# Kernel optimization log

Hardware: AMD Instinct MI355X
Metric: run time of the kernel (lower is better)

## Reference

```python
import jax, jax.numpy as jnp
import numpy as np
import math

B, S, D, H = 2, 2048, 1024, 16
D_K = D // H


def setup_inputs() -> dict:
    key = jax.random.key(0)
    ks = jax.random.split(key, 9)
    scale = 0.02
    return {
        "query": jax.random.normal(ks[0], (B, S, D), dtype=jnp.float32),
        "key": jax.random.normal(ks[1], (B, S, D), dtype=jnp.float32),
        "value": jax.random.normal(ks[2], (B, S, D), dtype=jnp.float32),
        "padding_mask": jax.random.bernoulli(ks[3], 0.1, (B, 1, 1, S)),
        "Wq": jax.random.normal(ks[4], (D, D), dtype=jnp.float32) * scale,
        "bq": jnp.zeros((D,), dtype=jnp.float32),
        "Wk": jax.random.normal(ks[5], (D, D), dtype=jnp.float32) * scale,
        "bk": jnp.zeros((D,), dtype=jnp.float32),
        "Wv": jax.random.normal(ks[6], (D, D), dtype=jnp.float32) * scale,
        "bv": jnp.zeros((D,), dtype=jnp.float32),
        "Wo": jax.random.normal(ks[7], (D, D), dtype=jnp.float32) * scale,
        "bo": jnp.zeros((D,), dtype=jnp.float32),
    }


def reference(query, key, value, padding_mask, Wq, bq, Wk, bk, Wv, bv, Wo, bo):
    # projections -> [B, H, S, d_k]
    q = (query @ Wq + bq).reshape(B, S, H, D_K).transpose(0, 2, 1, 3)
    k = (key @ Wk + bk).reshape(B, S, H, D_K).transpose(0, 2, 1, 3)
    v = (value @ Wv + bv).reshape(B, S, H, D_K).transpose(0, 2, 1, 3)

    # scores: [B, H, S, S]
    scores = jnp.einsum("bhqd,bhkd->bhqk", q, k) / math.sqrt(D_K)

    # faithful to original: triu(scores, 1).bool() -> True where upper-tri score != 0,
    # masked positions get value 1e-10 (NOT -inf) before softmax
    causal_mask = jnp.triu(scores, k=1) != 0
    scores = jnp.where(causal_mask, jnp.float32(1e-10), scores)
    scores = jnp.where(padding_mask, jnp.float32(1e-10), scores)

    attn = jax.nn.softmax(scores, axis=-1)
    out = jnp.einsum("bhqk,bhkd->bhqd", attn, v)  # [B, H, S, d_k]
    out = out.transpose(0, 2, 1, 3).reshape(B, S, D)
    return out @ Wo + bo
```

## Files before the change

### kernel.cpp

```cpp
#include <hip/hip_runtime.h>
#include <hip/hip_bf16.h>
#include <cstdint>
#include <cstddef>

typedef __hip_bfloat16 bf16;
typedef __attribute__((ext_vector_type(8))) short short8;
typedef __attribute__((ext_vector_type(4))) short s4v;
typedef __attribute__((ext_vector_type(4))) float floatx4;

#define B_ 2
#define S_ 2048
#define D_ 1024
#define H_ 16
#define DK_ 64
#define M_ 4096
#define HEADELEMS 131072
#define TILEELEMS 4096
#define QSCALE 0.1803368801111204f

struct __align__(8) bf16x4 { bf16 x, y, z, w; };

__device__ __forceinline__ floatx4 mfma16(short8 a, short8 b, floatx4 c) {
  return __builtin_amdgcn_mfma_f32_16x16x32_bf16(a, b, c, 0, 0, 0);
}
__device__ __forceinline__ void gl_lds16(const bf16* g, bf16* l) {
  __builtin_amdgcn_global_load_lds((const __attribute__((address_space(1))) void*)g,
                                   (__attribute__((address_space(3))) void*)l, 16, 0, 0);
}
__device__ __forceinline__ float bs2f(short s) {
  bf16 b = *reinterpret_cast<bf16*>(&s);
  return __bfloat162float(b);
}
__device__ __forceinline__ s4v pack4(float p0, float p1, float p2, float p3) {
  union { __hip_bfloat162 h; short2 s; } ua, ub;
  ua.h = __float22bfloat162_rn(make_float2(p0, p1));
  ub.h = __float22bfloat162_rn(make_float2(p2, p3));
  s4v r = {ua.s.x, ua.s.y, ub.s.x, ub.s.y};
  return r;
}
__device__ __forceinline__ float fast_exp2(float x) {
#if __has_builtin(__builtin_amdgcn_exp2f)
  return __builtin_amdgcn_exp2f(x);
#else
  float r; asm("v_exp_f32 %0, %1" : "=v"(r) : "v"(x)); return r;
#endif
}

__global__ void prep_kernel(const float* __restrict__ q_in, const float* __restrict__ k_in,
                            const float* __restrict__ v_in,
                            const float* __restrict__ Wq, const float* __restrict__ Wk,
                            const float* __restrict__ Wv, const float* __restrict__ Wo,
                            bf16* __restrict__ xq, bf16* __restrict__ xk, bf16* __restrict__ xv,
                            bf16* __restrict__ wqt, bf16* __restrict__ wkt,
                            bf16* __restrict__ wvt, bf16* __restrict__ wot,
                            const unsigned int* __restrict__ pmask, int* __restrict__ flag) {
  __shared__ bf16 tile[64][66];
  __shared__ int sbyte;
  const int blk = blockIdx.x;
  const int tid = threadIdx.x;
  if (blk < 12288) {
    const int z = blk >> 12;
    const int i = ((blk & 4095) << 8) | tid;
    const float* src = (z == 0) ? q_in : (z == 1) ? k_in : v_in;
    bf16* dst = (z == 0) ? xq : (z == 1) ? xk : xv;
    float4 v = ((const float4*)src)[i];
    bf16x4 o = { __float2bfloat16(v.x), __float2bfloat16(v.y),
                 __float2bfloat16(v.z), __float2bfloat16(v.w) };
    ((bf16x4*)dst)[i] = o;
  } else if (blk < 13312) {
    const int t = blk - 12288;
    const int z = t >> 8;
    const int rc = t & 255;
    const int r0 = (rc >> 4) * 64, c0 = (rc & 15) * 64;
    const float* src = (z == 0) ? Wq : (z == 1) ? Wk : (z == 2) ? Wv : Wo;
    bf16* dst = (z == 0) ? wqt : (z == 1) ? wkt : (z == 2) ? wvt : wot;
    const int lr = tid >> 4;
    const int lc4 = (tid & 15) * 4;
#pragma unroll
    for (int i = 0; i < 4; ++i) {
      const int r = lr + i * 16;
      float4 v = *(const float4*)(src + (size_t)(r0 + r) * D_ + c0 + lc4);
      tile[r][lc4 + 0] = __float2bfloat16(v.x);
      tile[r][lc4 + 1] = __float2bfloat16(v.y);
      tile[r][lc4 + 2] = __float2bfloat16(v.z);
      tile[r][lc4 + 3] = __float2bfloat16(v.w);
    }
    __syncthreads();
    const int orr = tid & 63;
    const int oc0 = tid >> 6;
#pragma unroll
    for (int j = 0; j < 16; ++j) {
      const int oc = oc0 + j * 4;
      dst[(size_t)(c0 + oc) * D_ + r0 + orr] = tile[orr][oc];
    }
  } else {
    if (tid == 0) sbyte = 0;
    __syncthreads();
    for (int i = tid; i < (B_ * S_) / 4; i += 256) {
      const unsigned int v = pmask[i];
      if (((v & 0xFEFEFEFEu) == 0u) && ((v & 0xFFFFFF00u) != 0u)) sbyte = 1;
    }
    __syncthreads();
    if (tid == 0) *flag = sbyte;
  }
}

template<int MT>
__global__ __launch_bounds__(256, 2) void gemm_k(
    const bf16* __restrict__ A0, const bf16* __restrict__ A1, const bf16* __restrict__ A2,
    const bf16* __restrict__ W0, const bf16* __restrict__ W1, const bf16* __restrict__ W2,
    const float* __restrict__ b0, const float* __restrict__ b1, const float* __restrict__ b2,
    void* __restrict__ O0, void* __restrict__ O1, void* __restrict__ O2,
    const int mode01, const int Kd, const float sc)
{
  constexpr int ROWS = MT + 128;
  __shared__ __align__(16) bf16 sh[2 * ROWS * 64];
  const int z = blockIdx.z;
  const bf16* A = (z == 0) ? A0 : (z == 1) ? A1 : A2;
  const bf16* W = (z == 0) ? W0 : (z == 1) ? W1 : W2;
  const float* bias = (z == 0) ? b0 : (z == 1) ? b1 : b2;
  void* Cout = (z == 0) ? O0 : (z == 1) ? O1 : O2;
  const int mode = (z == 2) ? 1 : mode01;
  const float scz = (z == 0) ? sc : 1.f;

  constexpr int MI = MT / 32;
  const int tid = threadIdx.x;
  const int wave = tid >> 6, lane = tid & 63;
  const int quad = lane >> 4, lc = lane & 15;
  const int wm = (wave >> 1) * (MT / 2), wn = (wave & 1) * 64;
  const int m0 = blockIdx.x * MT, n0 = blockIdx.y * 128;

  const floatx4 zero4 = {0.f, 0.f, 0.f, 0.f};
  floatx4 acc[MI][4];
#pragma unroll
  for (int mi = 0; mi < MI; ++mi)
#pragma unroll
    for (int ni = 0; ni < 4; ++ni) acc[mi][ni] = zero4;

  const int srow = lane >> 3;
  const int schunk = ((lane & 7) ^ srow) * 8;
  const bf16* Ag = A + (size_t)(m0 + wave * (MT / 4) + srow) * Kd + schunk;
  const bf16* Bg = W + (size_t)(n0 + wave * 32 + srow) * Kd + schunk;

  auto stage = [&](bf16* buf, int k0) {
    bf16* As0 = buf + wave * (MT / 4) * 64;
    bf16* Bs0 = buf + MT * 64 + wave * 32 * 64;
#pragma unroll
    for (int j = 0; j < MT / 32; ++j)
      gl_lds16(Ag + k0 + (size_t)(j * 8) * Kd, As0 + j * 512);
#pragma unroll
    for (int j = 0; j < 4; ++j)
      gl_lds16(Bg + k0 + (size_t)(j * 8) * Kd, Bs0 + j * 512);
  };

  stage(sh, 0);
  asm volatile("s_waitcnt vmcnt(0)" ::: "memory");
  __syncthreads();

  int cur = 0;
  for (int k0 = 0; k0 < Kd; k0 += 64) {
    bf16* cbuf = cur ? sh + ROWS * 64 : sh;
    bf16* nbuf = cur ? sh : sh + ROWS * 64;
    const bool more = (k0 + 64 < Kd);
    if (more) stage(nbuf, k0 + 64);

    const bf16* Ar = cbuf;
    const bf16* Br = cbuf + MT * 64;
    short8 af[2][MI], bfr[2][4];
#pragma unroll
    for (int kk = 0; kk < 2; ++kk) {
#pragma unroll
      for (int i = 0; i < MI; ++i)
        af[kk][i] = *(const short8*)(Ar + (wm + i * 16 + lc) * 64
                                     + (((kk * 4 + quad) ^ (lc & 7)) * 8));
#pragma unroll
      for (int i = 0; i < 4; ++i)
        bfr[kk][i] = *(const short8*)(Br + (wn + i * 16 + lc) * 64
                                      + (((kk * 4 + quad) ^ (lc & 7)) * 8));
    }
#pragma unroll
    for (int kk = 0; kk < 2; ++kk)
#pragma unroll
      for (int mi = 0; mi < MI; ++mi)
#pragma unroll
        for (int ni = 0; ni < 4; ++ni)
          acc[mi][ni] = mfma16(af[kk][mi], bfr[kk][ni], acc[mi][ni]);

    __syncthreads();
    cur ^= 1;
  }

  if (mode == 2) {
    float* out = (float*)Cout;
#pragma unroll
    for (int mi = 0; mi < MI; ++mi)
#pragma unroll
      for (int ni = 0; ni < 4; ++ni) {
        const int col = n0 + wn + ni * 16 + lc;
        const float bv = bias[col];
        const int rbase = m0 + wm + mi * 16 + quad * 4;
#pragma unroll
        for (int r = 0; r < 4; ++r)
          out[(size_t)(rbase + r) * D_ + col] = acc[mi][ni][r] + bv;
      }
  } else {
    bf16* pool = sh + wave * 2048;
    float bvs[4];
#pragma unroll
    for (int ni = 0; ni < 4; ++ni) bvs[ni] = bias[n0 + wn + ni * 16 + lc];
    const int hcol = (n0 + wn) >> 6;
    const int mglob = m0 + wm;
    bf16* outb = (bf16*)Cout + (size_t)((mglob >> 11) * H_ + hcol) * HEADELEMS
               + (size_t)((mglob & (S_ - 1)) >> 6) * TILEELEMS;
#pragma unroll
    for (int half = 0; half < MI / 2; ++half) {
#pragma unroll
      for (int mi2 = 0; mi2 < 2; ++mi2) {
        const int mi = half * 2 + mi2;
#pragma unroll
        for (int ni = 0; ni < 4; ++ni) {
          const int dkl = ni * 16 + lc;
#pragma unroll
          for (int r = 0; r < 4; ++r) {
            const float v = (acc[mi][ni][r] + bvs[ni]) * scz;
            int idx;
            if (mode == 0) {
              const int c = (mi2 * 2 + (dkl >> 5)) * 64 + ((dkl >> 3) & 3) * 16 + quad * 4 + r;
              idx = c * 8 + (dkl & 7);
            } else {
              const int c = (mi2 * 4 + (dkl >> 4)) * 64 + quad * 16 + (dkl & 15);
              idx = c * 4 + r;
            }
            pool[idx] = __float2bfloat16(v);
          }
        }
      }
#pragma unroll
      for (int t = 0; t < 4; ++t) {
        const short8 vv = *(const short8*)(pool + t * 512 + lane * 8);
        *(short8*)(outb + half * 2048 + t * 512 + lane * 8) = vv;
      }
    }
  }
}

__global__ void suf_kernel(const bf16* __restrict__ vp, float* __restrict__ suf) {
  __shared__ float ts[32 * 64];
  const int bhid = blockIdx.x;
  const bf16* vb = vp + (size_t)bhid * HEADELEMS;
  const int tid = threadIdx.x;
  const int dk = tid & 63, g = tid >> 6;
  const int dkt = dk >> 4, lck = dk & 15;
  for (int T = g * 8; T < g * 8 + 8; ++T) {
    float sum = 0.f;
#pragma unroll
    for (int w = 0; w < 4; ++w)
#pragma unroll
      for (int qd = 0; qd < 4; ++qd) {
        const s4v x = *(const s4v*)(vb + (size_t)T * TILEELEMS
                                    + (size_t)(((w * 4 + dkt) * 64 + qd * 16 + lck)) * 4);
        sum += bs2f(x[0]) + bs2f(x[1]) + bs2f(x[2]) + bs2f(x[3]);
      }
    ts[T * 64 + dk] = sum;
  }
  __syncthreads();
  if (g == 0) {
    float run = 0.f;
    float* out = suf + (size_t)bhid * (33 * 64);
    out[32 * 64 + dk] = 0.f;
    for (int T = 31; T >= 0; --T) { run += ts[T * 64 + dk]; out[T * 64 + dk] = run; }
  }
}

template<bool DIAGP>
__device__ __forceinline__ void qk_tile(const short8 ak0, const short8 ak1,
                                        const short8 (&qf)[4][2],
                                        const unsigned int (&pmb)[4], const int T,
                                        float (&lacc)[4], s4v (&pf)[4],
                                        const int w, const int quad, const int lc,
                                        const bool diag) {
  const floatx4 z4 = {0.f, 0.f, 0.f, 0.f};
  const short ONE = (short)0x3F80;
#pragma unroll
  for (int qt = 0; qt < 4; ++qt) {
    if (DIAGP && diag && w > qt) {
      s4v o1 = {ONE, ONE, ONE, ONE};
      pf[qt] = o1;
      lacc[qt] += 4.f;
      continue;
    }
    floatx4 s = mfma16(ak0, qf[qt][0], z4);
    s = mfma16(ak1, qf[qt][1], s);
    float pv[4];
#pragma unroll
    for (int r = 0; r < 4; ++r) {
      bool m = ((pmb[r] >> T) & 1u) != 0u;
      if (DIAGP && diag && w == qt) m = m || (quad * 4 + r > lc);
      pv[r] = fast_exp2(m ? 0.f : s[r]);
      lacc[qt] += pv[r];
    }
    pf[qt] = pack4(pv[0], pv[1], pv[2], pv[3]);
  }
}

__device__ __forceinline__ void pv_step(const s4v (&va0)[4], const s4v (&va1)[4],
                                        const s4v (&pf0)[4], const s4v (&pf1)[4],
                                        floatx4 (&oacc)[4][4]) {
  short8 pB[4];
#pragma unroll
  for (int qt = 0; qt < 4; ++qt)
    pB[qt] = __builtin_shufflevector(pf0[qt], pf1[qt], 0, 1, 2, 3, 4, 5, 6, 7);
#pragma unroll
  for (int dkt = 0; dkt < 4; ++dkt) {
    const short8 av = __builtin_shufflevector(va0[dkt], va1[dkt], 0, 1, 2, 3, 4, 5, 6, 7);
#pragma unroll
    for (int qt = 0; qt < 4; ++qt)
      oacc[dkt][qt] = mfma16(av, pB[qt], oacc[dkt][qt]);
  }
}

__device__ __forceinline__ void stage8(const bf16* kb, const bf16* vb, bf16* slot,
                                       const int T0, const int T1,
                                       const int wl, const int wreg) {
  const bf16* k0 = kb + (size_t)T0 * TILEELEMS + wl;
  const bf16* k1 = kb + (size_t)T1 * TILEELEMS + wl;
  const bf16* v0 = vb + (size_t)T0 * TILEELEMS + wl;
  const bf16* v1 = vb + (size_t)T1 * TILEELEMS + wl;
  gl_lds16(k0,       slot + wreg);
  gl_lds16(k0 + 512, slot + wreg + 512);
  gl_lds16(k1,       slot + 4096 + wreg);
  gl_lds16(k1 + 512, slot + 4096 + wreg + 512);
  gl_lds16(v0,       slot + 8192 + wreg);
  gl_lds16(v0 + 512, slot + 8192 + wreg + 512);
  gl_lds16(v1,       slot + 12288 + wreg);
  gl_lds16(v1 + 512, slot + 12288 + wreg + 512);
}

__global__ __launch_bounds__(256, 1) void attn_kernel(
    const bf16* __restrict__ qp, const bf16* __restrict__ kp,
    const bf16* __restrict__ vp, const float* __restrict__ suf,
    const void* __restrict__ pad, const int* __restrict__ flag,
    bf16* __restrict__ oa)
{
  __shared__ __align__(16) bf16 lds[32768];

  const int lin = blockIdx.x;
  const int xcd = lin & 7;
  const int t = lin >> 3;
  const int grp = t >> 4;
  const int jq = t & 15;
  const int bh = xcd + 8 * grp;
  const int b = bh >> 4, h = bh & 15;

  const int tid = threadIdx.x;
  const int w = tid >> 6, lane = tid & 63, quad = lane >> 4, lc = lane & 15;
  const int bytemode = *flag;

  const int wreg = w * 1024;
  const int wl = wreg + lane * 8;
  const int vl = wreg + lane * 4;

  const bf16* kb = kp + (size_t)bh * HEADELEMS;
  const bf16* vb = vp + (size_t)bh * HEADELEMS;

  unsigned int pmb[4] = {0u, 0u, 0u, 0u};
  if (bytemode) {
    const unsigned char* pp = (const unsigned char*)pad + b * S_ + w * 16 + quad * 4;
#pragma unroll
    for (int T = 0; T < 32; ++T) {
      const uchar4 u = *(const uchar4*)(pp + T * 64);
      pmb[0] |= (u.x ? 1u : 0u) << T;
      pmb[1] |= (u.y ? 1u : 0u) << T;
      pmb[2] |= (u.z ? 1u : 0u) << T;
      pmb[3] |= (u.w ? 1u : 0u) << T;
    }
  } else {
    const int* pp = (const int*)pad + b * S_ + w * 16 + quad * 4;
#pragma unroll
    for (int T = 0; T < 32; ++T) {
      const int4 u = *(const int4*)(pp + (size_t)T * 64);
      pmb[0] |= (u.x ? 1u : 0u) << T;
      pmb[1] |= (u.y ? 1u : 0u) << T;
      pmb[2] |= (u.z ? 1u : 0u) << T;
      pmb[3] |= (u.w ? 1u : 0u) << T;
    }
  }

#pragma unroll 1
  for (int qsel = 0; qsel < 2; ++qsel) {
    const int myqt = qsel ? jq : 31 - jq;
    const int mynt = myqt + 1;
    const int np = (mynt + 1) >> 1;

    const bf16* qb = qp + (size_t)bh * HEADELEMS + (size_t)myqt * TILEELEMS;
    gl_lds16(qb + wl,       lds + 16384 + wreg);
    gl_lds16(qb + wl + 512, lds + 16384 + wreg + 512);
    stage8(kb, vb, lds, 0, 1, wl, wreg);
    asm volatile("s_waitcnt vmcnt(0)" ::: "memory");
    __syncthreads();

    short8 qf[4][2];
#pragma unroll
    for (int qt = 0; qt < 4; ++qt)
#pragma unroll
      for (int hh = 0; hh < 2; ++hh)
        qf[qt][hh] = *(const short8*)(lds + 16384 + qt * 1024 + hh * 512 + lane * 8);
    __syncthreads();

    const floatx4 zero4 = {0.f, 0.f, 0.f, 0.f};
    floatx4 oacc[4][4];
#pragma unroll
    for (int i = 0; i < 4; ++i)
#pragma unroll
      for (int jj = 0; jj < 4; ++jj) oacc[i][jj] = zero4;
    float lacc[4] = {0.f, 0.f, 0.f, 0.f};

#pragma unroll 1
    for (int p = 0; p < np; ++p) {
      if (p + 1 < np) {
        stage8(kb, vb, lds + (((p + 1) & 1) << 14), 2 * p + 2, 2 * p + 3, wl, wreg);
        asm volatile("s_waitcnt vmcnt(8)" ::: "memory");
      } else {
        asm volatile("s_waitcnt vmcnt(0)" ::: "memory");
      }
      __builtin_amdgcn_sched_barrier(0);

      bf16* slot = lds + ((p & 1) << 14);
      const short8 ak00 = *(const short8*)(slot + wl);
      const short8 ak01 = *(const short8*)(slot + wl + 512);
      const short8 ak10 = *(const short8*)(slot + 4096 + wl);
      const short8 ak11 = *(const short8*)(slot + 4096 + wl + 512);
      s4v va0[4], va1[4];
#pragma unroll
      for (int dkt = 0; dkt < 4; ++dkt) {
        va0[dkt] = *(const s4v*)(slot + 8192 + vl + dkt * 256);
        va1[dkt] = *(const s4v*)(slot + 12288 + vl + dkt * 256);
      }

      const int T0 = 2 * p, T1 = 2 * p + 1;
      s4v pf0[4], pf1[4];
      if (p + 1 < np) {
        qk_tile<false>(ak00, ak01, qf, pmb, T0, lacc, pf0, w, quad, lc, false);
        qk_tile<false>(ak10, ak11, qf, pmb, T1, lacc, pf1, w, quad, lc, false);
      } else {
        qk_tile<true>(ak00, ak01, qf, pmb, T0, lacc, pf0, w, quad, lc, T0 == mynt - 1);
        if (T1 < mynt) {
          qk_tile<true>(ak10, ak11, qf, pmb, T1, lacc, pf1, w, quad, lc, true);
        } else {
          const s4v zz = {0, 0, 0, 0};
#pragma unroll
          for (int qt = 0; qt < 4; ++qt) pf1[qt] = zz;
        }
      }
      pv_step(va0, va1, pf0, pf1, oacc);
    }

    __syncthreads();

    float* fbuf = (float*)lds;
    bf16* obuf = lds + 8704;
    float* lbuf = (float*)(lds + 13312);

#pragma unroll
    for (int qt = 0; qt < 4; ++qt) {
      float v = lacc[qt];
      v += __shfl_xor(v, 16);
      v += __shfl_xor(v, 32);
      if (quad == 0) lbuf[w * 64 + qt * 16 + lc] = v;
    }
    __syncthreads();
    float ls = lbuf[0 * 64 + w * 16 + lc] + lbuf[1 * 64 + w * 16 + lc]
             + lbuf[2 * 64 + w * 16 + lc] + lbuf[3 * 64 + w * 16 + lc];
    ls += (float)(S_ - mynt * 64);
    const float linv = 1.f / ls;
    const float* sufp = suf + (size_t)bh * (33 * 64) + mynt * 64;

#pragma unroll
    for (int dktG = 0; dktG < 4; ++dktG) {
#pragma unroll
      for (int qt = 0; qt < 4; ++qt) {
        const floatx4 a = oacc[dktG][qt];
        float* dst = fbuf + (w * 4 + qt) * 272 + lc;
#pragma unroll
        for (int r = 0; r < 4; ++r) dst[(quad * 4 + r) * 17] = a[r];
      }
      __syncthreads();
      const float4 sv4 = *(const float4*)(sufp + dktG * 16 + quad * 4);
      float v[4];
#pragma unroll
      for (int r = 0; r < 4; ++r) {
        const int e = (quad * 4 + r) * 17 + lc;
        v[r] = fbuf[(0 * 4 + w) * 272 + e] + fbuf[(1 * 4 + w) * 272 + e]
             + fbuf[(2 * 4 + w) * 272 + e] + fbuf[(3 * 4 + w) * 272 + e];
      }
      v[0] = (v[0] + sv4.x) * linv; v[1] = (v[1] + sv4.y) * linv;
      v[2] = (v[2] + sv4.z) * linv; v[3] = (v[3] + sv4.w) * linv;
      bf16x4 pk = { __float2bfloat16(v[0]), __float2bfloat16(v[1]),
                    __float2bfloat16(v[2]), __float2bfloat16(v[3]) };
      *(bf16x4*)(obuf + (w * 16 + lc) * 72 + dktG * 16 + quad * 4) = pk;
      __syncthreads();
    }

    const size_t obase = (size_t)(b * S_ + myqt * 64) * D_ + h * 64;
#pragma unroll
    for (int it = 0; it < 2; ++it) {
      const int idx = it * 256 + tid;
      const int row = idx >> 3, c8 = (idx & 7) * 8;
      const short8 vv = *(const short8*)(obuf + row * 72 + c8);
      *(short8*)(oa + obase + (size_t)row * D_ + c8) = vv;
    }
    __syncthreads();
  }
}

extern "C" void kernel_launch(void* const* d_in, const int* in_sizes, int n_in,
                              void* d_out, int out_size, void* d_ws, size_t ws_size,
                              hipStream_t stream) {
  (void)in_sizes; (void)n_in; (void)out_size; (void)ws_size;
  const float* q_in = (const float*)d_in[0];
  const float* k_in = (const float*)d_in[1];
  const float* v_in = (const float*)d_in[2];
  const void*  pmask = d_in[3];
  const float* Wq = (const float*)d_in[4];
  const float* bq = (const float*)d_in[5];
  const float* Wk = (const float*)d_in[6];
  const float* bk = (const float*)d_in[7];
  const float* Wv = (const float*)d_in[8];
  const float* bv = (const float*)d_in[9];
  const float* Wo = (const float*)d_in[10];
  const float* bo = (const float*)d_in[11];

  char* ws = (char*)d_ws;
  bf16* xq  = (bf16*)(ws + 0);
  bf16* xk  = (bf16*)(ws + 8388608);
  bf16* xv  = (bf16*)(ws + 16777216);
  bf16* wqt = (bf16*)(ws + 25165824);
  bf16* wkt = (bf16*)(ws + 27262976);
  bf16* wvt = (bf16*)(ws + 29360128);
  bf16* wot = (bf16*)(ws + 31457280);
  bf16* qpp = (bf16*)(ws + 33554432);
  bf16* kpp = (bf16*)(ws + 41943040);
  bf16* vpp = (bf16*)(ws + 50331648);
  float* suf = (float*)(ws + 25165824);
  int*  flg = (int*)(ws + 58720256);
  bf16* oa  = xq;

  prep_kernel<<<13313, 256, 0, stream>>>(q_in, k_in, v_in, Wq, Wk, Wv, Wo,
                                         xq, xk, xv, wqt, wkt, wvt, wot,
                                         (const unsigned int*)pmask, flg);

  gemm_k<128><<<dim3(32, 8, 3), 256, 0, stream>>>(xq, xk, xv, wqt, wkt, wvt,
                                                  bq, bk, bv, qpp, kpp, vpp, 0, D_, QSCALE);
  suf_kernel<<<32, 256, 0, stream>>>(vpp, suf);

  attn_kernel<<<512, 256, 0, stream>>>(qpp, kpp, vpp, suf, pmask, flg, oa);

  gemm_k<128><<<dim3(32, 8, 1), 256, 0, stream>>>(oa, oa, oa, wot, wot, wot,
                                                  bo, bo, bo, d_out, d_out, d_out, 2, D_, 1.f);
}
```

Measured before the change: 216.3 us.

## Compute softmax row sums via MFMA and split K/V waits in attention loop

Replaces the per-lane scalar accumulation of softmax denominators with an extra MFMA against a ones vector, so the sums fall out of the matrix unit and the cross-lane shuffles at the end go away. The P tile is built directly in the MFMA operand layout instead of being shuffled together afterwards. The wait on staged loads is split so QK^T can start once the K tiles arrive while the V tiles are still in flight. Launch bounds now allow two blocks per CU, which may constrain register allocation. Masked entries now map directly to one instead of exp2(0).

```diff
diff --git a/kernel.cpp b/kernel.cpp
--- a/kernel.cpp
+++ b/kernel.cpp
@@ -276,17 +276,19 @@
 __device__ __forceinline__ void qk_tile(const short8 ak0, const short8 ak1,
                                         const short8 (&qf)[4][2],
                                         const unsigned int (&pmb)[4], const int T,
-                                        float (&lacc)[4], s4v (&pf)[4],
+                                        short8 (&pB)[4], const int half,
                                         const int w, const int quad, const int lc,
                                         const bool diag) {
   const floatx4 z4 = {0.f, 0.f, 0.f, 0.f};
   const short ONE = (short)0x3F80;
+  bool mm[4];
+#pragma unroll
+  for (int r = 0; r < 4; ++r) mm[r] = ((pmb[r] >> T) & 1u) != 0u;
 #pragma unroll
   for (int qt = 0; qt < 4; ++qt) {
     if (DIAGP && diag && w > qt) {
       s4v o1 = {ONE, ONE, ONE, ONE};
-      pf[qt] = o1;
-      lacc[qt] += 4.f;
+      ((s4v*)&pB[qt])[half] = o1;
       continue;
     }
     floatx4 s = mfma16(ak0, qf[qt][0], z4);
@@ -294,29 +296,24 @@
     float pv[4];
 #pragma unroll
     for (int r = 0; r < 4; ++r) {
-      bool m = ((pmb[r] >> T) & 1u) != 0u;
+      bool m = mm[r];
       if (DIAGP && diag && w == qt) m = m || (quad * 4 + r > lc);
-      pv[r] = fast_exp2(m ? 0.f : s[r]);
-      lacc[qt] += pv[r];
-    }
-    pf[qt] = pack4(pv[0], pv[1], pv[2], pv[3]);
-  }
-}
-
-__device__ __forceinline__ void pv_step(const s4v (&va0)[4], const s4v (&va1)[4],
-                                        const s4v (&pf0)[4], const s4v (&pf1)[4],
+      pv[r] = m ? 1.f : fast_exp2(s[r]);
+    }
+    ((s4v*)&pB[qt])[half] = pack4(pv[0], pv[1], pv[2], pv[3]);
+  }
+}
+
+__device__ __forceinline__ void pv_step(const short8 (&av)[4], const short8 (&pB)[4],
+                                        const short8 ones, floatx4 (&lsum)[4],
                                         floatx4 (&oacc)[4][4]) {
-  short8 pB[4];
-#pragma unroll
-  for (int qt = 0; qt < 4; ++qt)
-    pB[qt] = __builtin_shufflevector(pf0[qt], pf1[qt], 0, 1, 2, 3, 4, 5, 6, 7);
-#pragma unroll
-  for (int dkt = 0; dkt < 4; ++dkt) {
-    const short8 av = __builtin_shufflevector(va0[dkt], va1[dkt], 0, 1, 2, 3, 4, 5, 6, 7);
+#pragma unroll
+  for (int qt = 0; qt < 4; ++qt) lsum[qt] = mfma16(ones, pB[qt], lsum[qt]);
+#pragma unroll
+  for (int dkt = 0; dkt < 4; ++dkt)
 #pragma unroll
     for (int qt = 0; qt < 4; ++qt)
-      oacc[dkt][qt] = mfma16(av, pB[qt], oacc[dkt][qt]);
-  }
+      oacc[dkt][qt] = mfma16(av[dkt], pB[qt], oacc[dkt][qt]);
 }
 
 __device__ __forceinline__ void stage8(const bf16* kb, const bf16* vb, bf16* slot,
@@ -336,7 +333,7 @@
   gl_lds16(v1 + 512, slot + 12288 + wreg + 512);
 }
 
-__global__ __launch_bounds__(256, 1) void attn_kernel(
+__global__ __launch_bounds__(256, 2) void attn_kernel(
     const bf16* __restrict__ qp, const bf16* __restrict__ kp,
     const bf16* __restrict__ vp, const float* __restrict__ suf,
     const void* __restrict__ pad, const int* __restrict__ flag,
@@ -363,6 +360,9 @@
   const bf16* kb = kp + (size_t)bh * HEADELEMS;
   const bf16* vb = vp + (size_t)bh * HEADELEMS;
 
+  const short ONE = (short)0x3F80;
+  const short8 ones = {ONE, ONE, ONE, ONE, ONE, ONE, ONE, ONE};
+
   unsigned int pmb[4] = {0u, 0u, 0u, 0u};
   if (bytemode) {
     const unsigned char* pp = (const unsigned char*)pad + b * S_ + w * 16 + quad * 4;
@@ -413,15 +413,16 @@
     for (int i = 0; i < 4; ++i)
 #pragma unroll
       for (int jj = 0; jj < 4; ++jj) oacc[i][jj] = zero4;
-    float lacc[4] = {0.f, 0.f, 0.f, 0.f};
+    floatx4 lsum[4] = {zero4, zero4, zero4, zero4};
 
 #pragma unroll 1
     for (int p = 0; p < np; ++p) {
-      if (p + 1 < np) {
+      const bool more = (p + 1 < np);
+      if (more) {
         stage8(kb, vb, lds + (((p + 1) & 1) << 14), 2 * p + 2, 2 * p + 3, wl, wreg);
-        asm volatile("s_waitcnt vmcnt(8)" ::: "memory");
+        asm volatile("s_waitcnt vmcnt(12)" ::: "memory");
       } else {
-        asm volatile("s_waitcnt vmcnt(0)" ::: "memory");
+        asm volatile("s_waitcnt vmcnt(4)" ::: "memory");
       }
       __builtin_amdgcn_sched_barrier(0);
 
@@ -430,29 +431,34 @@
       const short8 ak01 = *(const short8*)(slot + wl + 512);
       const short8 ak10 = *(const short8*)(slot + 4096 + wl);
       const short8 ak11 = *(const short8*)(slot + 4096 + wl + 512);
-      s4v va0[4], va1[4];
-#pragma unroll
-      for (int dkt = 0; dkt < 4; ++dkt) {
-        va0[dkt] = *(const s4v*)(slot + 8192 + vl + dkt * 256);
-        va1[dkt] = *(const s4v*)(slot + 12288 + vl + dkt * 256);
-      }
 
       const int T0 = 2 * p, T1 = 2 * p + 1;
-      s4v pf0[4], pf1[4];
-      if (p + 1 < np) {
-        qk_tile<false>(ak00, ak01, qf, pmb, T0, lacc, pf0, w, quad, lc, false);
-        qk_tile<false>(ak10, ak11, qf, pmb, T1, lacc, pf1, w, quad, lc, false);
+      short8 pB[4];
+      if (more) {
+        qk_tile<false>(ak00, ak01, qf, pmb, T0, pB, 0, w, quad, lc, false);
+        qk_tile<false>(ak10, ak11, qf, pmb, T1, pB, 1, w, quad, lc, false);
       } else {
-        qk_tile<true>(ak00, ak01, qf, pmb, T0, lacc, pf0, w, quad, lc, T0 == mynt - 1);
+        qk_tile<true>(ak00, ak01, qf, pmb, T0, pB, 0, w, quad, lc, T0 == mynt - 1);
         if (T1 < mynt) {
-          qk_tile<true>(ak10, ak11, qf, pmb, T1, lacc, pf1, w, quad, lc, true);
+          qk_tile<true>(ak10, ak11, qf, pmb, T1, pB, 1, w, quad, lc, true);
         } else {
           const s4v zz = {0, 0, 0, 0};
 #pragma unroll
-          for (int qt = 0; qt < 4; ++qt) pf1[qt] = zz;
+          for (int qt = 0; qt < 4; ++qt) ((s4v*)&pB[qt])[1] = zz;
         }
       }
-      pv_step(va0, va1, pf0, pf1, oacc);
+
+      if (more) asm volatile("s_waitcnt vmcnt(8)" ::: "memory");
+      else      asm volatile("s_waitcnt vmcnt(0)" ::: "memory");
+      __builtin_amdgcn_sched_barrier(0);
+
+      short8 av[4];
+#pragma unroll
+      for (int dkt = 0; dkt < 4; ++dkt) {
+        ((s4v*)&av[dkt])[0] = *(const s4v*)(slot + 8192 + vl + dkt * 256);
+        ((s4v*)&av[dkt])[1] = *(const s4v*)(slot + 12288 + vl + dkt * 256);
+      }
+      pv_step(av, pB, ones, lsum, oacc);
     }
 
     __syncthreads();
@@ -462,12 +468,8 @@
     float* lbuf = (float*)(lds + 13312);
 
 #pragma unroll
-    for (int qt = 0; qt < 4; ++qt) {
-      float v = lacc[qt];
-      v += __shfl_xor(v, 16);
-      v += __shfl_xor(v, 32);
-      if (quad == 0) lbuf[w * 64 + qt * 16 + lc] = v;
-    }
+    for (int qt = 0; qt < 4; ++qt)
+      if (quad == 0) lbuf[w * 64 + qt * 16 + lc] = lsum[qt][0];
     __syncthreads();
     float ls = lbuf[0 * 64 + w * 16 + lc] + lbuf[1 * 64 + w * 16 + lc]
              + lbuf[2 * 64 + w * 16 + lc] + lbuf[3 * 64 + w * 16 + lc];
```

Result: slower. 221.4 us (+2.4%).

## Split attention block into 8 waves with per-tile 4-stage K/V pipeline

Applied to the files above, without the earlier changes.

The attention kernel goes from 256 to 512 threads per block. Each wave now owns one key sub-tile and half of the query tiles, which halves the per-wave accumulator state. Staging changes from two-tile double buffering to a 4-slot ring of single 64-key tiles: half the waves load K and half load V, and PV MFMAs run on pairs of tiles. The aim is more waves in flight to hide latency and lower register pressure, at the cost of more barriers per tile and a reworked reduction epilogue.

```diff
diff --git a/kernel.cpp b/kernel.cpp
--- a/kernel.cpp
+++ b/kernel.cpp
@@ -19,6 +19,7 @@
 #define QSCALE 0.1803368801111204f
 
 struct __align__(8) bf16x4 { bf16 x, y, z, w; };
+struct __align__(4) bf16x2 { bf16 x, y; };
 
 __device__ __forceinline__ floatx4 mfma16(short8 a, short8 b, floatx4 c) {
   return __builtin_amdgcn_mfma_f32_16x16x32_bf16(a, b, c, 0, 0, 0);
@@ -213,10 +214,10 @@
     bf16* outb = (bf16*)Cout + (size_t)((mglob >> 11) * H_ + hcol) * HEADELEMS
                + (size_t)((mglob & (S_ - 1)) >> 6) * TILEELEMS;
 #pragma unroll
-    for (int half = 0; half < MI / 2; ++half) {
+    for (int half2 = 0; half2 < MI / 2; ++half2) {
 #pragma unroll
       for (int mi2 = 0; mi2 < 2; ++mi2) {
-        const int mi = half * 2 + mi2;
+        const int mi = half2 * 2 + mi2;
 #pragma unroll
         for (int ni = 0; ni < 4; ++ni) {
           const int dkl = ni * 16 + lc;
@@ -238,7 +239,7 @@
 #pragma unroll
       for (int t = 0; t < 4; ++t) {
         const short8 vv = *(const short8*)(pool + t * 512 + lane * 8);
-        *(short8*)(outb + half * 2048 + t * 512 + lane * 8) = vv;
+        *(short8*)(outb + half2 * 2048 + t * 512 + lane * 8) = vv;
       }
     }
   }
@@ -273,19 +274,20 @@
 }
 
 template<bool DIAGP>
-__device__ __forceinline__ void qk_tile(const short8 ak0, const short8 ak1,
-                                        const short8 (&qf)[4][2],
-                                        const unsigned int (&pmb)[4], const int T,
-                                        float (&lacc)[4], s4v (&pf)[4],
-                                        const int w, const int quad, const int lc,
-                                        const bool diag) {
+__device__ __forceinline__ void qk2(const short8 ak0, const short8 ak1,
+                                    const short8 (&qf)[2][2],
+                                    const unsigned int (&pmb)[4], const int T,
+                                    short8 (&pB)[2], float (&lacc)[2], const int hlf,
+                                    const int kw, const int qh,
+                                    const int quad, const int lc, const bool diag) {
   const floatx4 z4 = {0.f, 0.f, 0.f, 0.f};
   const short ONE = (short)0x3F80;
 #pragma unroll
-  for (int qt = 0; qt < 4; ++qt) {
-    if (DIAGP && diag && w > qt) {
+  for (int qt = 0; qt < 2; ++qt) {
+    const int qtg = qh * 2 + qt;
+    if (DIAGP && diag && kw > qtg) {
       s4v o1 = {ONE, ONE, ONE, ONE};
-      pf[qt] = o1;
+      ((s4v*)&pB[qt])[hlf] = o1;
       lacc[qt] += 4.f;
       continue;
     }
@@ -295,48 +297,15 @@
 #pragma unroll
     for (int r = 0; r < 4; ++r) {
       bool m = ((pmb[r] >> T) & 1u) != 0u;
-      if (DIAGP && diag && w == qt) m = m || (quad * 4 + r > lc);
-      pv[r] = fast_exp2(m ? 0.f : s[r]);
+      if (DIAGP && diag && kw == qtg) m = m || (quad * 4 + r > lc);
+      pv[r] = m ? 1.f : fast_exp2(s[r]);
       lacc[qt] += pv[r];
     }
-    pf[qt] = pack4(pv[0], pv[1], pv[2], pv[3]);
-  }
-}
-
-__device__ __forceinline__ void pv_step(const s4v (&va0)[4], const s4v (&va1)[4],
-                                        const s4v (&pf0)[4], const s4v (&pf1)[4],
-                                        floatx4 (&oacc)[4][4]) {
-  short8 pB[4];
-#pragma unroll
-  for (int qt = 0; qt < 4; ++qt)
-    pB[qt] = __builtin_shufflevector(pf0[qt], pf1[qt], 0, 1, 2, 3, 4, 5, 6, 7);
-#pragma unroll
-  for (int dkt = 0; dkt < 4; ++dkt) {
-    const short8 av = __builtin_shufflevector(va0[dkt], va1[dkt], 0, 1, 2, 3, 4, 5, 6, 7);
-#pragma unroll
-    for (int qt = 0; qt < 4; ++qt)
-      oacc[dkt][qt] = mfma16(av, pB[qt], oacc[dkt][qt]);
-  }
-}
-
-__device__ __forceinline__ void stage8(const bf16* kb, const bf16* vb, bf16* slot,
-                                       const int T0, const int T1,
-                                       const int wl, const int wreg) {
-  const bf16* k0 = kb + (size_t)T0 * TILEELEMS + wl;
-  const bf16* k1 = kb + (size_t)T1 * TILEELEMS + wl;
-  const bf16* v0 = vb + (size_t)T0 * TILEELEMS + wl;
-  const bf16* v1 = vb + (size_t)T1 * TILEELEMS + wl;
-  gl_lds16(k0,       slot + wreg);
-  gl_lds16(k0 + 512, slot + wreg + 512);
-  gl_lds16(k1,       slot + 4096 + wreg);
-  gl_lds16(k1 + 512, slot + 4096 + wreg + 512);
-  gl_lds16(v0,       slot + 8192 + wreg);
-  gl_lds16(v0 + 512, slot + 8192 + wreg + 512);
-  gl_lds16(v1,       slot + 12288 + wreg);
-  gl_lds16(v1 + 512, slot + 12288 + wreg + 512);
-}
-
-__global__ __launch_bounds__(256, 1) void attn_kernel(
+    ((s4v*)&pB[qt])[hlf] = pack4(pv[0], pv[1], pv[2], pv[3]);
+  }
+}
+
+__global__ __launch_bounds__(512, 4) void attn_kernel(
     const bf16* __restrict__ qp, const bf16* __restrict__ kp,
     const bf16* __restrict__ vp, const float* __restrict__ suf,
     const void* __restrict__ pad, const int* __restrict__ flag,
@@ -354,18 +323,18 @@
 
   const int tid = threadIdx.x;
   const int w = tid >> 6, lane = tid & 63, quad = lane >> 4, lc = lane & 15;
+  const int kw = w & 3, qh = w >> 2;
   const int bytemode = *flag;
-
-  const int wreg = w * 1024;
-  const int wl = wreg + lane * 8;
-  const int vl = wreg + lane * 4;
 
   const bf16* kb = kp + (size_t)bh * HEADELEMS;
   const bf16* vb = vp + (size_t)bh * HEADELEMS;
+  const bf16* stgsrc = qh ? vb : kb;
+  const int stgoff = kw * 1024;
+  const int stgdst = (qh ? 4096 : 0) + kw * 1024;
 
   unsigned int pmb[4] = {0u, 0u, 0u, 0u};
   if (bytemode) {
-    const unsigned char* pp = (const unsigned char*)pad + b * S_ + w * 16 + quad * 4;
+    const unsigned char* pp = (const unsigned char*)pad + b * S_ + kw * 16 + quad * 4;
 #pragma unroll
     for (int T = 0; T < 32; ++T) {
       const uchar4 u = *(const uchar4*)(pp + T * 64);
@@ -375,7 +344,7 @@
       pmb[3] |= (u.w ? 1u : 0u) << T;
     }
   } else {
-    const int* pp = (const int*)pad + b * S_ + w * 16 + quad * 4;
+    const int* pp = (const int*)pad + b * S_ + kw * 16 + quad * 4;
 #pragma unroll
     for (int T = 0; T < 32; ++T) {
       const int4 u = *(const int4*)(pp + (size_t)T * 64);
@@ -390,69 +359,88 @@
   for (int qsel = 0; qsel < 2; ++qsel) {
     const int myqt = qsel ? jq : 31 - jq;
     const int mynt = myqt + 1;
-    const int np = (mynt + 1) >> 1;
 
     const bf16* qb = qp + (size_t)bh * HEADELEMS + (size_t)myqt * TILEELEMS;
-    gl_lds16(qb + wl,       lds + 16384 + wreg);
-    gl_lds16(qb + wl + 512, lds + 16384 + wreg + 512);
-    stage8(kb, vb, lds, 0, 1, wl, wreg);
-    asm volatile("s_waitcnt vmcnt(0)" ::: "memory");
-    __syncthreads();
-
-    short8 qf[4][2];
-#pragma unroll
-    for (int qt = 0; qt < 4; ++qt)
+    bf16* qarea = lds + 3 * 8192;
+    gl_lds16(qb + w * 512 + lane * 8, qarea + w * 512);
+    {
+      const bf16* s0 = stgsrc + stgoff + lane * 8;
+      gl_lds16(s0, lds + stgdst);
+      gl_lds16(s0 + 512, lds + stgdst + 512);
+      if (mynt > 1) {
+        const bf16* s1 = stgsrc + (size_t)TILEELEMS + stgoff + lane * 8;
+        gl_lds16(s1, lds + 8192 + stgdst);
+        gl_lds16(s1 + 512, lds + 8192 + stgdst + 512);
+      }
+    }
+    if (mynt > 1) asm volatile("s_waitcnt vmcnt(4)" ::: "memory");
+    else          asm volatile("s_waitcnt vmcnt(2)" ::: "memory");
+    __builtin_amdgcn_s_barrier();
+    __builtin_amdgcn_sched_barrier(0);
+
+    short8 qf[2][2];
+#pragma unroll
+    for (int qt = 0; qt < 2; ++qt)
 #pragma unroll
       for (int hh = 0; hh < 2; ++hh)
-        qf[qt][hh] = *(const short8*)(lds + 16384 + qt * 1024 + hh * 512 + lane * 8);
-    __syncthreads();
+        qf[qt][hh] = *(const short8*)(qarea + (qh * 2 + qt) * 1024 + hh * 512 + lane * 8);
+    asm volatile("s_waitcnt lgkmcnt(0)" ::: "memory");
+    __builtin_amdgcn_sched_barrier(0);
+    __builtin_amdgcn_s_barrier();
 
     const floatx4 zero4 = {0.f, 0.f, 0.f, 0.f};
-    floatx4 oacc[4][4];
+    floatx4 oacc[4][2];
 #pragma unroll
     for (int i = 0; i < 4; ++i)
 #pragma unroll
-      for (int jj = 0; jj < 4; ++jj) oacc[i][jj] = zero4;
-    float lacc[4] = {0.f, 0.f, 0.f, 0.f};
+      for (int jj = 0; jj < 2; ++jj) oacc[i][jj] = zero4;
+    float lacc[2] = {0.f, 0.f};
+    short8 pB[2];
 
 #pragma unroll 1
-    for (int p = 0; p < np; ++p) {
-      if (p + 1 < np) {
-        stage8(kb, vb, lds + (((p + 1) & 1) << 14), 2 * p + 2, 2 * p + 3, wl, wreg);
-        asm volatile("s_waitcnt vmcnt(8)" ::: "memory");
-      } else {
-        asm volatile("s_waitcnt vmcnt(0)" ::: "memory");
-      }
+    for (int T = 0; T < mynt; ++T) {
+      if (T + 1 < mynt) asm volatile("s_waitcnt vmcnt(2)" ::: "memory");
+      else              asm volatile("s_waitcnt vmcnt(0)" ::: "memory");
+      __builtin_amdgcn_s_barrier();
       __builtin_amdgcn_sched_barrier(0);
 
-      bf16* slot = lds + ((p & 1) << 14);
-      const short8 ak00 = *(const short8*)(slot + wl);
-      const short8 ak01 = *(const short8*)(slot + wl + 512);
-      const short8 ak10 = *(const short8*)(slot + 4096 + wl);
-      const short8 ak11 = *(const short8*)(slot + 4096 + wl + 512);
-      s4v va0[4], va1[4];
-#pragma unroll
-      for (int dkt = 0; dkt < 4; ++dkt) {
-        va0[dkt] = *(const s4v*)(slot + 8192 + vl + dkt * 256);
-        va1[dkt] = *(const s4v*)(slot + 12288 + vl + dkt * 256);
-      }
-
-      const int T0 = 2 * p, T1 = 2 * p + 1;
-      s4v pf0[4], pf1[4];
-      if (p + 1 < np) {
-        qk_tile<false>(ak00, ak01, qf, pmb, T0, lacc, pf0, w, quad, lc, false);
-        qk_tile<false>(ak10, ak11, qf, pmb, T1, lacc, pf1, w, quad, lc, false);
-      } else {
-        qk_tile<true>(ak00, ak01, qf, pmb, T0, lacc, pf0, w, quad, lc, T0 == mynt - 1);
-        if (T1 < mynt) {
-          qk_tile<true>(ak10, ak11, qf, pmb, T1, lacc, pf1, w, quad, lc, true);
-        } else {
+      if (T + 2 < mynt) {
+        bf16* sl = lds + (((T + 2) & 3) << 13) + stgdst;
+        const bf16* src = stgsrc + (size_t)(T + 2) * TILEELEMS + stgoff + lane * 8;
+        gl_lds16(src, sl);
+        gl_lds16(src + 512, sl + 512);
+      }
+
+      const bf16* slot = lds + ((T & 3) << 13);
+      const short8 ak0 = *(const short8*)(slot + kw * 1024 + lane * 8);
+      const short8 ak1 = *(const short8*)(slot + kw * 1024 + 512 + lane * 8);
+
+      const int hlf = T & 1;
+      const bool diag = (T == mynt - 1);
+      if (!diag) qk2<false>(ak0, ak1, qf, pmb, T, pB, lacc, hlf, kw, qh, quad, lc, false);
+      else       qk2<true >(ak0, ak1, qf, pmb, T, pB, lacc, hlf, kw, qh, quad, lc, true);
+
+      if (hlf == 1 || diag) {
+        if (diag && hlf == 0) {
           const s4v zz = {0, 0, 0, 0};
 #pragma unroll
-          for (int qt = 0; qt < 4; ++qt) pf1[qt] = zz;
+          for (int qt = 0; qt < 2; ++qt) ((s4v*)&pB[qt])[1] = zz;
         }
-      }
-      pv_step(va0, va1, pf0, pf1, oacc);
+        const int Te = T & ~1;
+        const bf16* se = lds + ((Te & 3) << 13);
+        const bf16* so = (hlf == 1) ? slot : se;
+        short8 av[4];
+#pragma unroll
+        for (int dkt = 0; dkt < 4; ++dkt) {
+          ((s4v*)&av[dkt])[0] = *(const s4v*)(se + 4096 + kw * 1024 + dkt * 256 + lane * 4);
+          ((s4v*)&av[dkt])[1] = *(const s4v*)(so + 4096 + kw * 1024 + dkt * 256 + lane * 4);
+        }
+#pragma unroll
+        for (int dkt = 0; dkt < 4; ++dkt)
+#pragma unroll
+          for (int qt = 0; qt < 2; ++qt)
+            oacc[dkt][qt] = mfma16(av[dkt], pB[qt], oacc[dkt][qt]);
+      }
     }
 
     __syncthreads();
@@ -462,15 +450,17 @@
     float* lbuf = (float*)(lds + 13312);
 
 #pragma unroll
-    for (int qt = 0; qt < 4; ++qt) {
+    for (int qt = 0; qt < 2; ++qt) {
       float v = lacc[qt];
       v += __shfl_xor(v, 16);
       v += __shfl_xor(v, 32);
-      if (quad == 0) lbuf[w * 64 + qt * 16 + lc] = v;
-    }
-    __syncthreads();
-    float ls = lbuf[0 * 64 + w * 16 + lc] + lbuf[1 * 64 + w * 16 + lc]
-             + lbuf[2 * 64 + w * 16 + lc] + lbuf[3 * 64 + w * 16 + lc];
+      if (quad == 0) lbuf[(qh * 2 + qt) * 64 + kw * 16 + lc] = v;
+    }
+    __syncthreads();
+    const int qtgR = w & 3;
+    const int rh = w >> 2;
+    float ls = lbuf[qtgR * 64 + 0 * 16 + lc] + lbuf[qtgR * 64 + 1 * 16 + lc]
+             + lbuf[qtgR * 64 + 2 * 16 + lc] + lbuf[qtgR * 64 + 3 * 16 + lc];
     ls += (float)(S_ - mynt * 64);
     const float linv = 1.f / ls;
     const float* sufp = suf + (size_t)bh * (33 * 64) + mynt * 64;
@@ -478,34 +468,31 @@
 #pragma unroll
     for (int dktG = 0; dktG < 4; ++dktG) {
 #pragma unroll
-      for (int qt = 0; qt < 4; ++qt) {
+      for (int qt = 0; qt < 2; ++qt) {
         const floatx4 a = oacc[dktG][qt];
-        float* dst = fbuf + (w * 4 + qt) * 272 + lc;
+        float* dst = fbuf + (qh * 2 + qt) * 1088 + kw * 272 + lc;
 #pragma unroll
         for (int r = 0; r < 4; ++r) dst[(quad * 4 + r) * 17] = a[r];
       }
       __syncthreads();
-      const float4 sv4 = *(const float4*)(sufp + dktG * 16 + quad * 4);
-      float v[4];
-#pragma unroll
-      for (int r = 0; r < 4; ++r) {
-        const int e = (quad * 4 + r) * 17 + lc;
-        v[r] = fbuf[(0 * 4 + w) * 272 + e] + fbuf[(1 * 4 + w) * 272 + e]
-             + fbuf[(2 * 4 + w) * 272 + e] + fbuf[(3 * 4 + w) * 272 + e];
-      }
-      v[0] = (v[0] + sv4.x) * linv; v[1] = (v[1] + sv4.y) * linv;
-      v[2] = (v[2] + sv4.z) * linv; v[3] = (v[3] + sv4.w) * linv;
-      bf16x4 pk = { __float2bfloat16(v[0]), __float2bfloat16(v[1]),
-                    __float2bfloat16(v[2]), __float2bfloat16(v[3]) };
-      *(bf16x4*)(obuf + (w * 16 + lc) * 72 + dktG * 16 + quad * 4) = pk;
+      const float2 sv = *(const float2*)(sufp + dktG * 16 + rh * 8 + quad * 2);
+      float v0, v1;
+      {
+        const int e0 = qtgR * 1088 + (rh * 8 + quad * 2 + 0) * 17 + lc;
+        const int e1 = qtgR * 1088 + (rh * 8 + quad * 2 + 1) * 17 + lc;
+        v0 = fbuf[e0] + fbuf[e0 + 272] + fbuf[e0 + 544] + fbuf[e0 + 816];
+        v1 = fbuf[e1] + fbuf[e1 + 272] + fbuf[e1 + 544] + fbuf[e1 + 816];
+      }
+      v0 = (v0 + sv.x) * linv;
+      v1 = (v1 + sv.y) * linv;
+      bf16x2 pk = { __float2bfloat16(v0), __float2bfloat16(v1) };
+      *(bf16x2*)(obuf + (qtgR * 16 + lc) * 72 + dktG * 16 + rh * 8 + quad * 2) = pk;
       __syncthreads();
     }
 
     const size_t obase = (size_t)(b * S_ + myqt * 64) * D_ + h * 64;
-#pragma unroll
-    for (int it = 0; it < 2; ++it) {
-      const int idx = it * 256 + tid;
-      const int row = idx >> 3, c8 = (idx & 7) * 8;
+    {
+      const int row = tid >> 3, c8 = (tid & 7) * 8;
       const short8 vv = *(const short8*)(obuf + row * 72 + c8);
       *(short8*)(oa + obase + (size_t)row * D_ + c8) = vv;
     }
@@ -553,7 +540,7 @@
                                                   bq, bk, bv, qpp, kpp, vpp, 0, D_, QSCALE);
   suf_kernel<<<32, 256, 0, stream>>>(vpp, suf);
 
-  attn_kernel<<<512, 256, 0, stream>>>(qpp, kpp, vpp, suf, pmask, flg, oa);
+  attn_kernel<<<512, 512, 0, stream>>>(qpp, kpp, vpp, suf, pmask, flg, oa);
 
   gemm_k<128><<<dim3(32, 8, 1), 256, 0, stream>>>(oa, oa, oa, wot, wot, wot,
                                                   bo, bo, bo, d_out, d_out, d_out, 2, D_, 1.f);
```

Result: slower. 290.9 us (+34.5%).
